# Kernel optimization log

Measured on AMD Instinct MI355X. Metric: run time of the kernel, lower is better.

## Reference

```python
import jax, jax.numpy as jnp
import numpy as np

N_EMBED = 768
N_HEAD = 12
SEQ = 4096
BATCH = 1
LN_EPS = 1e-5


def setup_inputs() -> dict:
    key = jax.random.key(0)
    ks = jax.random.split(key, 12)
    d = N_EMBED
    s = 0.02
    return {
        "x": jax.random.normal(ks[0], (BATCH, SEQ, d), jnp.float32),
        "w_qkv": jax.random.normal(ks[1], (d, 3 * d), jnp.float32) * s,
        "b_qkv": jnp.zeros((3 * d,), jnp.float32),
        "w_proj": jax.random.normal(ks[2], (d, d), jnp.float32) * s,
        "b_proj": jnp.zeros((d,), jnp.float32),
        "w_fc1": jax.random.normal(ks[3], (d, 4 * d), jnp.float32) * s,
        "b_fc1": jnp.zeros((4 * d,), jnp.float32),
        "w_fc2": jax.random.normal(ks[4], (4 * d, d), jnp.float32) * s,
        "b_fc2": jnp.zeros((d,), jnp.float32),
        "ln1_g": jnp.ones((d,), jnp.float32),
        "ln1_b": jnp.zeros((d,), jnp.float32),
        "ln2_g": jnp.ones((d,), jnp.float32),
        "ln2_b": jnp.zeros((d,), jnp.float32),
    }


def _layernorm(x, g, b):
    mu = jnp.mean(x, axis=-1, keepdims=True)
    var = jnp.mean(jnp.square(x - mu), axis=-1, keepdims=True)
    return (x - mu) * jax.lax.rsqrt(var + LN_EPS) * g + b


def _attn(x, w_qkv, b_qkv, w_proj, b_proj):
    B, S, D = x.shape
    hd = D // N_HEAD
    kqv = x @ w_qkv + b_qkv
    # torch order: k, q, v
    k, q, v = jnp.split(kqv, 3, axis=-1)
    def heads(t):
        return t.reshape(B, S, N_HEAD, hd).transpose(0, 2, 1, 3)  # [B,H,S,hd]
    k, q, v = heads(k), heads(q), heads(v)
    scores = jnp.einsum("bhqd,bhkd->bhqk", q, k) * (1.0 / jnp.sqrt(jnp.float32(hd)))
    causal = jnp.tril(jnp.ones((S, S), bool))
    scores = jnp.where(causal, scores, -jnp.inf)
    attn = jax.nn.softmax(scores, axis=-1)
    # dropout is identity in eval mode
    y = jnp.einsum("bhqk,bhkd->bhqd", attn, v)
    y = y.transpose(0, 2, 1, 3).reshape(B, S, D)
    return y @ w_proj + b_proj


def reference(x, w_qkv, b_qkv, w_proj, b_proj, w_fc1, b_fc1, w_fc2, b_fc2,
              ln1_g, ln1_b, ln2_g, ln2_b):
    x = x + _attn(_layernorm(x, ln1_g, ln1_b), w_qkv, b_qkv, w_proj, b_proj)
    h = _layernorm(x, ln2_g, ln2_b)
    h = jax.nn.gelu(h @ w_fc1 + b_fc1, approximate=False)
    return x + (h @ w_fc2 + b_fc2)
```

## Files before the change

### kernel.cpp

```cpp
#include <hip/hip_runtime.h>
#include <hip/hip_bf16.h>

#define S_LEN 4096
#define D_EMB 768
#define NH    12
#define HD    64
#define DQKV  2304
#define DFF   3072

typedef __attribute__((ext_vector_type(4))) short short4v;
typedef __attribute__((ext_vector_type(8))) short short8v;
typedef __attribute__((ext_vector_type(4))) float float4v;

static __device__ __forceinline__ float4v mfma16(short4v a, short4v b, float4v c) {
  return __builtin_amdgcn_mfma_f32_16x16x16bf16_1k(a, b, c, 0, 0, 0);
}

static __device__ __forceinline__ short bf16bits(float f) {
  __hip_bfloat16 h = __float2bfloat16(f);
  return *reinterpret_cast<short*>(&h);
}

static __device__ __forceinline__ float fast_exp2(float x) {
#if __has_builtin(__builtin_amdgcn_exp2f)
  return __builtin_amdgcn_exp2f(x);
#else
  return exp2f(x);
#endif
}

static __device__ __forceinline__ void gload16(const __hip_bfloat16* g, __hip_bfloat16* l) {
  __builtin_amdgcn_global_load_lds((const __attribute__((address_space(1))) void*)g,
                                   (__attribute__((address_space(3))) void*)l, 16, 0, 0);
}

__global__ __launch_bounds__(256) void ln_kernel(const float* __restrict__ x,
    const float* __restrict__ g, const float* __restrict__ b,
    __hip_bfloat16* __restrict__ out)
{
  int row = blockIdx.x;
  int tid = threadIdx.x;
  const float* xr = x + (size_t)row * D_EMB;
  float v0 = xr[tid], v1 = xr[tid + 256], v2 = xr[tid + 512];
  float s  = v0 + v1 + v2;
  float sq = v0 * v0 + v1 * v1 + v2 * v2;
  #pragma unroll
  for (int off = 32; off >= 1; off >>= 1) {
    s  += __shfl_xor(s, off);
    sq += __shfl_xor(sq, off);
  }
  __shared__ float ss[4], ssq[4];
  if ((tid & 63) == 0) { ss[tid >> 6] = s; ssq[tid >> 6] = sq; }
  __syncthreads();
  s  = ss[0] + ss[1] + ss[2] + ss[3];
  sq = ssq[0] + ssq[1] + ssq[2] + ssq[3];
  float mean = s * (1.0f / D_EMB);
  float var  = sq * (1.0f / D_EMB) - mean * mean;
  float rstd = rsqrtf(var + 1e-5f);
  __hip_bfloat16* orow = out + (size_t)row * D_EMB;
  orow[tid]       = __float2bfloat16((v0 - mean) * rstd * g[tid]       + b[tid]);
  orow[tid + 256] = __float2bfloat16((v1 - mean) * rstd * g[tid + 256] + b[tid + 256]);
  orow[tid + 512] = __float2bfloat16((v2 - mean) * rstd * g[tid + 512] + b[tid + 512]);
}

__global__ __launch_bounds__(256) void transpose_bf16_kernel(const float* __restrict__ in,
    __hip_bfloat16* __restrict__ out, int K, int N)
{
  __shared__ float t[32][33];
  int nb = N >> 5;
  int bn = blockIdx.x % nb, bk = blockIdx.x / nb;
  int tx = threadIdx.x & 31, ty = threadIdx.x >> 5;
  #pragma unroll
  for (int i = 0; i < 4; i++)
    t[ty + 8 * i][tx] = in[(size_t)(bk * 32 + ty + 8 * i) * N + bn * 32 + tx];
  __syncthreads();
  #pragma unroll
  for (int i = 0; i < 4; i++)
    out[(size_t)(bn * 32 + ty + 8 * i) * K + bk * 32 + tx] = __float2bfloat16(t[tx][ty + 8 * i]);
}

template<int EPI>
__global__ __launch_bounds__(256) void gemm_kernel(
    const __hip_bfloat16* __restrict__ A,
    const __hip_bfloat16* __restrict__ Bt,
    const float* __restrict__ bias,
    const float* __restrict__ resid,
    void* __restrict__ Cout,
    __hip_bfloat16* __restrict__ vtout,
    int M, int N, int Kfull, int kChunk)
{
  __shared__ __hip_bfloat16 Asm[128 * 64];
  __shared__ __hip_bfloat16 Bsm[128 * 64];
  int nb = N >> 7, mb = M >> 7;
  int tilesPer = nb * mb;
  int split = blockIdx.x / tilesPer;
  int b2 = blockIdx.x % tilesPer;
  int bx = b2 % nb, by = b2 / nb;
  int m0 = by << 7, n0 = bx << 7;
  int k0 = split * kChunk;
  int tid = threadIdx.x;
  int lane = tid & 63, lg = lane >> 4, li = lane & 15;
  int w = tid >> 6, wr = w >> 1, wc = w & 1;

  int sr  = tid >> 3;
  int scn = (tid & 7) ^ (sr & 7);
  const __hip_bfloat16* aSrc = A  + (size_t)(m0 + sr) * Kfull + k0 + scn * 8;
  const __hip_bfloat16* bSrc = Bt + (size_t)(n0 + sr) * Kfull + k0 + scn * 8;
  __hip_bfloat16* aDst = Asm + tid * 8;
  __hip_bfloat16* bDst = Bsm + tid * 8;
  const size_t rowStep = (size_t)32 * Kfull;

  float4v acc[4][4];
  #pragma unroll
  for (int i = 0; i < 4; i++)
    #pragma unroll
    for (int j = 0; j < 4; j++) {
      float4v z = {0.f, 0.f, 0.f, 0.f};
      acc[i][j] = z;
    }

  int sw = li & 7;

  for (int kt = 0; kt < kChunk; kt += 64) {
    #pragma unroll
    for (int i = 0; i < 4; i++) {
      gload16(aSrc + i * rowStep, aDst + i * 2048);
      gload16(bSrc + i * rowStep, bDst + i * 2048);
    }
    aSrc += 64; bSrc += 64;
    __syncthreads();
    #pragma unroll
    for (int kk = 0; kk < 2; kk++) {
      short8v af[4], bf[4];
      #pragma unroll
      for (int f = 0; f < 4; f++) {
        int ar = wr * 64 + f * 16 + li;
        int br = wc * 64 + f * 16 + li;
        int ch = ((kk << 2) | lg) ^ sw;
        af[f] = *(const short8v*)(Asm + ar * 64 + ch * 8);
        bf[f] = *(const short8v*)(Bsm + br * 64 + ch * 8);
      }
      #pragma unroll
      for (int fr = 0; fr < 4; fr++)
        #pragma unroll
        for (int fc = 0; fc < 4; fc++)
          acc[fr][fc] = __builtin_amdgcn_mfma_f32_16x16x32_bf16(af[fr], bf[fc], acc[fr][fc], 0, 0, 0);
    }
    __syncthreads();
  }

  #pragma unroll
  for (int fr = 0; fr < 4; fr++) {
    int row = m0 + wr * 64 + fr * 16 + lg * 4;
    #pragma unroll
    for (int fc = 0; fc < 4; fc++) {
      int col = n0 + wc * 64 + fc * 16 + li;
      float bv = (EPI == 3) ? 0.f : bias[col];
      short4v tv;
      #pragma unroll
      for (int r = 0; r < 4; r++) {
        float v = acc[fr][fc][r] + bv;
        size_t idx = (size_t)(row + r) * N + col;
        if (EPI == 1) {
          float u = 0.7978845608028654f * (v + 0.044715f * v * v * v);
          float e = fast_exp2(u * 2.8853900817779268f);
#if __has_builtin(__builtin_amdgcn_rcpf)
          float r1 = __builtin_amdgcn_rcpf(e + 1.0f);
#else
          float r1 = 1.0f / (e + 1.0f);
#endif
          v = v * e * r1;
          ((__hip_bfloat16*)Cout)[idx] = __float2bfloat16(v);
        } else if (EPI == 2) {
          ((float*)Cout)[idx] = v + resid[idx];
        } else if (EPI == 3) {
          ((__hip_bfloat16*)Cout)[(size_t)split * M * N + idx] = __float2bfloat16(v);
        } else {
          __hip_bfloat16 hb = __float2bfloat16(v);
          ((__hip_bfloat16*)Cout)[idx] = hb;
          if (EPI == 4) tv[r] = *reinterpret_cast<short*>(&hb);
        }
      }
      if (EPI == 4 && col >= 2 * D_EMB) {
        *reinterpret_cast<short4v*>(vtout + (size_t)(col - 2 * D_EMB) * S_LEN + row) = tv;
      }
    }
  }
}

template<int NS>
__global__ __launch_bounds__(256) void reduce_kernel(const __hip_bfloat16* __restrict__ parts,
    const float* __restrict__ bias, const float* __restrict__ resid,
    float* __restrict__ out, int n4)
{
  const size_t MN = (size_t)S_LEN * D_EMB;
  int stride = gridDim.x * 256;
  for (int e = blockIdx.x * 256 + threadIdx.x; e < n4; e += stride) {
    float4v acc = *(const float4v*)(resid + 4 * (size_t)e);
    int col = (e * 4) % D_EMB;
    float4v bv = *(const float4v*)(bias + col);
    acc += bv;
    #pragma unroll
    for (int s = 0; s < NS; s++) {
      short4v pv = *(const short4v*)(parts + (size_t)s * MN + 4 * (size_t)e);
      #pragma unroll
      for (int j = 0; j < 4; j++) {
        unsigned int u = ((unsigned int)(unsigned short)pv[j]) << 16;
        acc[j] += *reinterpret_cast<float*>(&u);
      }
    }
    *(float4v*)(out + 4 * (size_t)e) = acc;
  }
}

__global__ __launch_bounds__(256) void reduce_ln_kernel(const __hip_bfloat16* __restrict__ parts,
    const float* __restrict__ bias, const float* __restrict__ resid,
    const float* __restrict__ g, const float* __restrict__ b,
    float* __restrict__ x1, __hip_bfloat16* __restrict__ lnout)
{
  const size_t MN = (size_t)S_LEN * D_EMB;
  int row = blockIdx.x;
  int tid = threadIdx.x;
  float v[3];
  float s = 0.f, sq = 0.f;
  #pragma unroll
  for (int i = 0; i < 3; i++) {
    int col = tid + i * 256;
    size_t idx = (size_t)row * D_EMB + col;
    float a = resid[idx] + bias[col]
            + __bfloat162float(parts[idx])
            + __bfloat162float(parts[idx + MN])
            + __bfloat162float(parts[idx + 2 * MN]);
    x1[idx] = a;
    v[i] = a;
    s += a;
    sq += a * a;
  }
  #pragma unroll
  for (int off = 32; off >= 1; off >>= 1) {
    s  += __shfl_xor(s, off);
    sq += __shfl_xor(sq, off);
  }
  __shared__ float ss[4], ssq[4];
  if ((tid & 63) == 0) { ss[tid >> 6] = s; ssq[tid >> 6] = sq; }
  __syncthreads();
  s  = ss[0] + ss[1] + ss[2] + ss[3];
  sq = ssq[0] + ssq[1] + ssq[2] + ssq[3];
  float mean = s * (1.0f / D_EMB);
  float var  = sq * (1.0f / D_EMB) - mean * mean;
  float rstd = rsqrtf(var + 1e-5f);
  __hip_bfloat16* orow = lnout + (size_t)row * D_EMB;
  #pragma unroll
  for (int i = 0; i < 3; i++) {
    int col = tid + i * 256;
    orow[col] = __float2bfloat16((v[i] - mean) * rstd * g[col] + b[col]);
  }
}

#define SCL_LOG2E 0.18033688011f
template<bool SPLIT>
__global__ __launch_bounds__(512, 4) void attn_kernel(const __hip_bfloat16* __restrict__ kqv,
                                                      const __hip_bfloat16* __restrict__ vT,
                                                      __hip_bfloat16* __restrict__ y,
                                                      char* __restrict__ partial)
{
  __shared__ __hip_bfloat16 Ksm[2][64 * 64];
  __shared__ __hip_bfloat16 Vtsm[2][64 * 64];

  int bid = blockIdx.x;
  int h, gi, c;
  if (SPLIT) {
    int task = (bid >> 3) + (bid & 7) * 60;
    h = task / 40;
    int t = task % 40;
    if      (t < 16) { gi = 15 - (t >> 2);        c = t & 3; }
    else if (t < 28) { gi = 11 - (t - 16) / 3;    c = (t - 16) % 3; }
    else if (t < 36) { gi = 7  - ((t - 28) >> 1); c = (t - 28) & 1; }
    else             { gi = 3  - (t - 36);        c = 0; }
  } else {
    h = bid / 16; gi = 15 - (bid % 16); c = 0;
  }
  int ntile = 4 * gi + 4;
  int kt0 = c << 4;
  int kt1 = SPLIT ? min(kt0 + 16, ntile) : ntile;
  bool direct = SPLIT ? (gi < 4) : true;

  int tid = threadIdx.x;
  int w = tid >> 6, lane = tid & 63, lg = lane >> 4, li = lane & 15;
  int sw = li & 7;
  int qb0 = gi * 256 + w * 16;

  int ksr  = tid >> 3;
  int kscn = (tid & 7) ^ (ksr & 7);
  const __hip_bfloat16* kSrc0 = kqv + h * HD + (size_t)ksr * DQKV + kscn * 8;
  const __hip_bfloat16* vSrc0 = vT + (size_t)(h * HD + ksr) * S_LEN + kscn * 8;
  const size_t kTileStep = (size_t)64 * DQKV;

  short8v q8[2][2];
  #pragma unroll
  for (int g = 0; g < 2; g++) {
    const __hip_bfloat16* qp = kqv + (size_t)(qb0 + g * 128 + li) * DQKV + D_EMB + h * HD + 8 * lg;
    q8[g][0] = *(const short8v*)(qp);
    q8[g][1] = *(const short8v*)(qp + 32);
  }

  const short4v ones4 = { (short)0x3F80, (short)0x3F80, (short)0x3F80, (short)0x3F80 };
  float4v ol0 = {0.f,0.f,0.f,0.f}, ol1 = {0.f,0.f,0.f,0.f};
  float4v o0[4], o1[4];
  #pragma unroll
  for (int fc = 0; fc < 4; fc++) { float4v z = {0.f,0.f,0.f,0.f}; o0[fc] = z; o1[fc] = z; }

  gload16(kSrc0 + (size_t)kt0 * kTileStep, Ksm[0] + tid * 8);
  gload16(vSrc0 + (size_t)kt0 * 64,        Vtsm[0] + tid * 8);

  for (int kb = kt0; kb < kt1; kb++) {
    int p = kb & 1;
    __syncthreads();
    if (kb + 1 < kt1) {
      gload16(kSrc0 + (size_t)(kb + 1) * kTileStep, Ksm[p ^ 1] + tid * 8);
      gload16(vSrc0 + (size_t)(kb + 1) * 64,        Vtsm[p ^ 1] + tid * 8);
    }

    bool act0 = (kb * 64 <= qb0 + 15);
    bool act1 = (kb * 64 <= qb0 + 128 + 15);
    if (!act1) continue;

    float4v s0[4], s1[4];
    #pragma unroll
    for (int fc = 0; fc < 4; fc++) { float4v z = {0.f,0.f,0.f,0.f}; s0[fc] = z; s1[fc] = z; }
    #pragma unroll
    for (int kk = 0; kk < 2; kk++) {
      #pragma unroll
      for (int fc = 0; fc < 4; fc++) {
        int ch = ((kk << 2) | lg) ^ sw;
        short8v kf = *(const short8v*)(Ksm[p] + (fc * 16 + li) * 64 + ch * 8);
        s0[fc] = __builtin_amdgcn_mfma_f32_16x16x32_bf16(kf, q8[0][kk], s0[fc], 0, 0, 0);
        s1[fc] = __builtin_amdgcn_mfma_f32_16x16x32_bf16(kf, q8[1][kk], s1[fc], 0, 0, 0);
      }
    }

    if (act0) {
      bool needmask = (kb * 64 + 63 > qb0);
      if (needmask) {
        #pragma unroll
        for (int fc = 0; fc < 4; fc++) {
          #pragma unroll
          for (int rr = 0; rr < 4; rr++) {
            float pv = fast_exp2(s0[fc][rr] * SCL_LOG2E);
            if ((kb * 64 + fc * 16 + 4 * lg + rr) > (qb0 + li)) pv = 0.f;
            s0[fc][rr] = pv;
          }
        }
      } else {
        #pragma unroll
        for (int fc = 0; fc < 4; fc++) {
          #pragma unroll
          for (int rr = 0; rr < 4; rr++)
            s0[fc][rr] = fast_exp2(s0[fc][rr] * SCL_LOG2E);
        }
      }
    }

    {
      int qb1 = qb0 + 128;
      bool needmask = (kb * 64 + 63 > qb1);
      if (needmask) {
        #pragma unroll
        for (int fc = 0; fc < 4; fc++) {
          #pragma unroll
          for (int rr = 0; rr < 4; rr++) {
            float pv = fast_exp2(s1[fc][rr] * SCL_LOG2E);
            if ((kb * 64 + fc * 16 + 4 * lg + rr) > (qb1 + li)) pv = 0.f;
            s1[fc][rr] = pv;
          }
        }
      } else {
        #pragma unroll
        for (int fc = 0; fc < 4; fc++) {
          #pragma unroll
          for (int rr = 0; rr < 4; rr++)
            s1[fc][rr] = fast_exp2(s1[fc][rr] * SCL_LOG2E);
        }
      }
    }

    if (act0) {
      #pragma unroll
      for (int kk = 0; kk < 4; kk++) {
        short4v pb0, pb1;
        #pragma unroll
        for (int rr = 0; rr < 4; rr++) { pb0[rr] = bf16bits(s0[kk][rr]); pb1[rr] = bf16bits(s1[kk][rr]); }
        ol0 = mfma16(ones4, pb0, ol0);
        ol1 = mfma16(ones4, pb1, ol1);
        int c2 = (kk << 1) | (lg >> 1);
        #pragma unroll
        for (int fc = 0; fc < 4; fc++) {
          short4v vf = *(const short4v*)(Vtsm[p] + (fc * 16 + li) * 64 + ((c2 ^ sw) << 3) + 4 * (lg & 1));
          o0[fc] = mfma16(vf, pb0, o0[fc]);
          o1[fc] = mfma16(vf, pb1, o1[fc]);
        }
      }
    } else {
      #pragma unroll
      for (int kk = 0; kk < 4; kk++) {
        short4v pb1;
        #pragma unroll
        for (int rr = 0; rr < 4; rr++) pb1[rr] = bf16bits(s1[kk][rr]);
        ol1 = mfma16(ones4, pb1, ol1);
        int c2 = (kk << 1) | (lg >> 1);
        #pragma unroll
        for (int fc = 0; fc < 4; fc++) {
          short4v vf = *(const short4v*)(Vtsm[p] + (fc * 16 + li) * 64 + ((c2 ^ sw) << 3) + 4 * (lg & 1));
          o1[fc] = mfma16(vf, pb1, o1[fc]);
        }
      }
    }
  }

  if (direct) {
    float inv0 = 1.0f / ol0[0], inv1 = 1.0f / ol1[0];
    int q0 = qb0 + li;
    #pragma unroll
    for (int fc = 0; fc < 4; fc++) {
      short4v ov0, ov1;
      #pragma unroll
      for (int rr = 0; rr < 4; rr++) { ov0[rr] = bf16bits(o0[fc][rr] * inv0); ov1[rr] = bf16bits(o1[fc][rr] * inv1); }
      *reinterpret_cast<short4v*>(y + (size_t)q0 * D_EMB + h * HD + fc * 16 + 4 * lg) = ov0;
      *reinterpret_cast<short4v*>(y + (size_t)(q0 + 128) * D_EMB + h * HD + fc * 16 + 4 * lg) = ov1;
    }
  } else {
    int offg = (gi < 8) ? (gi - 4) * 2 : (gi < 12) ? 8 + (gi - 8) * 3 : 20 + (gi - 12) * 4;
    char* slot = partial + (size_t)(h * 36 + offg + c) * 33792;
    int q = (w & 3) * 16 + li;
    #pragma unroll
    for (int g = 0; g < 2; g++) {
      char* ps = slot + (size_t)(g * 2 + (w >> 2)) * 8448;
      __hip_bfloat16* pO = (__hip_bfloat16*)ps;
      float* pL = (float*)(ps + 8192);
      #pragma unroll
      for (int fc = 0; fc < 4; fc++) {
        #pragma unroll
        for (int rr = 0; rr < 4; rr++) {
          float val = g ? o1[fc][rr] : o0[fc][rr];
          pO[(fc * 16 + 4 * lg + rr) * 64 + q] = __float2bfloat16(val);
        }
      }
      if (lg == 0) pL[q] = g ? ol1[0] : ol0[0];
    }
  }
}

__global__ __launch_bounds__(256) void attn_combine_kernel(const char* __restrict__ partial,
                                                           __hip_bfloat16* __restrict__ y)
{
  int task = blockIdx.x;
  int h  = task / 48;
  int qb = 16 + task % 48;
  int gi = qb >> 2, slab = qb & 3;
  int nch = (gi >> 2) + 1;
  int offg = (gi < 8) ? (gi - 4) * 2 : (gi < 12) ? 8 + (gi - 8) * 3 : 20 + (gi - 12) * 4;
  const char* base = partial + (size_t)(h * 36 + offg) * 33792 + (size_t)slab * 8448;
  int wv = threadIdx.x >> 6;
  int lane = threadIdx.x & 63;

  float L = 0.f;
  float acc[16];
  #pragma unroll
  for (int j = 0; j < 16; j++) acc[j] = 0.f;
  #pragma unroll
  for (int c = 0; c < 4; c++) {
    if (c < nch) {
      const char* cb = base + (size_t)c * 33792;
      L += ((const float*)(cb + 8192))[lane];
      const __hip_bfloat16* O = (const __hip_bfloat16*)cb;
      #pragma unroll
      for (int j = 0; j < 16; j++)
        acc[j] += __bfloat162float(O[(wv * 16 + j) * 64 + lane]);
    }
  }
  float inv = 1.0f / L;
  __hip_bfloat16* yp = y + (size_t)(qb * 64 + lane) * D_EMB + h * HD + wv * 16;
  short8v a0, a1;
  #pragma unroll
  for (int j = 0; j < 8; j++) a0[j] = bf16bits(acc[j] * inv);
  #pragma unroll
  for (int j = 0; j < 8; j++) a1[j] = bf16bits(acc[8 + j] * inv);
  *reinterpret_cast<short8v*>(yp)     = a0;
  *reinterpret_cast<short8v*>(yp + 8) = a1;
}

extern "C" void kernel_launch(void* const* d_in, const int* in_sizes, int n_in,
                              void* d_out, int out_size, void* d_ws, size_t ws_size,
                              hipStream_t stream)
{
  const float* x      = (const float*)d_in[0];
  const float* w_qkv  = (const float*)d_in[1];
  const float* b_qkv  = (const float*)d_in[2];
  const float* w_proj = (const float*)d_in[3];
  const float* b_proj = (const float*)d_in[4];
  const float* w_fc1  = (const float*)d_in[5];
  const float* b_fc1  = (const float*)d_in[6];
  const float* w_fc2  = (const float*)d_in[7];
  const float* b_fc2  = (const float*)d_in[8];
  const float* ln1_g  = (const float*)d_in[9];
  const float* ln1_b  = (const float*)d_in[10];
  const float* ln2_g  = (const float*)d_in[11];
  const float* ln2_b  = (const float*)d_in[12];

  char* ws = (char*)d_ws;
  size_t off = 0;
  __hip_bfloat16* wqkvT = (__hip_bfloat16*)(ws + off); off += (size_t)DQKV * D_EMB * 2;
  __hip_bfloat16* wprojT= (__hip_bfloat16*)(ws + off); off += (size_t)D_EMB * D_EMB * 2;
  __hip_bfloat16* wfc1T = (__hip_bfloat16*)(ws + off); off += (size_t)DFF * D_EMB * 2;
  __hip_bfloat16* wfc2T = (__hip_bfloat16*)(ws + off); off += (size_t)D_EMB * DFF * 2;
  __hip_bfloat16* lnbuf = (__hip_bfloat16*)(ws + off); off += (size_t)S_LEN * D_EMB * 2;
  __hip_bfloat16* kqv   = (__hip_bfloat16*)(ws + off);
  __hip_bfloat16* hbuf  = kqv;                         off += (size_t)S_LEN * DQKV * 2;
  __hip_bfloat16* ybuf  = (__hip_bfloat16*)(ws + off); off += (size_t)S_LEN * D_EMB * 2;
  __hip_bfloat16* vTbuf = (__hip_bfloat16*)(ws + off); off += (size_t)S_LEN * D_EMB * 2;
  float*          x1    = (float*)(ws + off);          off += (size_t)S_LEN * D_EMB * 4;
  char*           part  = ws + off;
  size_t needSplit = off + (size_t)4 * S_LEN * D_EMB * 2;
  size_t needAttn  = off + (size_t)432 * 33792;
  bool splitk  = (ws_size >= needSplit);
  bool attnSpl = (ws_size >= needAttn);
  const int MN4 = S_LEN * D_EMB / 4;
  (void)in_sizes; (void)n_in; (void)out_size;

  transpose_bf16_kernel<<<dim3((DQKV/32)*(D_EMB/32)), dim3(256), 0, stream>>>(w_qkv,  wqkvT, D_EMB, DQKV);
  transpose_bf16_kernel<<<dim3((D_EMB/32)*(D_EMB/32)), dim3(256), 0, stream>>>(w_proj, wprojT, D_EMB, D_EMB);
  transpose_bf16_kernel<<<dim3((DFF/32)*(D_EMB/32)),   dim3(256), 0, stream>>>(w_fc1,  wfc1T, D_EMB, DFF);
  transpose_bf16_kernel<<<dim3((D_EMB/32)*(DFF/32)),   dim3(256), 0, stream>>>(w_fc2,  wfc2T, DFF, D_EMB);

  ln_kernel<<<dim3(S_LEN), dim3(256), 0, stream>>>(x, ln1_g, ln1_b, lnbuf);
  gemm_kernel<4><<<dim3((DQKV/128)*(S_LEN/128)), dim3(256), 0, stream>>>(
      lnbuf, wqkvT, b_qkv, nullptr, kqv, vTbuf, S_LEN, DQKV, D_EMB, D_EMB);

  if (attnSpl) {
    attn_kernel<true><<<dim3(480), dim3(512), 0, stream>>>(kqv, vTbuf, ybuf, part);
    attn_combine_kernel<<<dim3(576), dim3(256), 0, stream>>>(part, ybuf);
  } else {
    attn_kernel<false><<<dim3(192), dim3(512), 0, stream>>>(kqv, vTbuf, ybuf, part);
  }

  if (splitk) {
    gemm_kernel<3><<<dim3((D_EMB/128)*(S_LEN/128)*3), dim3(256), 0, stream>>>(
        ybuf, wprojT, nullptr, nullptr, part, nullptr, S_LEN, D_EMB, D_EMB, D_EMB/3);
    reduce_ln_kernel<<<dim3(S_LEN), dim3(256), 0, stream>>>(
        (const __hip_bfloat16*)part, b_proj, x, ln2_g, ln2_b, x1, lnbuf);
  } else {
    gemm_kernel<2><<<dim3((D_EMB/128)*(S_LEN/128)), dim3(256), 0, stream>>>(
        ybuf, wprojT, b_proj, x, x1, nullptr, S_LEN, D_EMB, D_EMB, D_EMB);
    ln_kernel<<<dim3(S_LEN), dim3(256), 0, stream>>>(x1, ln2_g, ln2_b, lnbuf);
  }

  gemm_kernel<1><<<dim3((DFF/128)*(S_LEN/128)), dim3(256), 0, stream>>>(
      lnbuf, wfc1T, b_fc1, nullptr, hbuf, nullptr, S_LEN, DFF, D_EMB, D_EMB);

  if (splitk) {
    gemm_kernel<3><<<dim3((D_EMB/128)*(S_LEN/128)*4), dim3(256), 0, stream>>>(
        hbuf, wfc2T, nullptr, nullptr, part, nullptr, S_LEN, D_EMB, DFF, DFF/4);
    reduce_kernel<4><<<dim3(1024), dim3(256), 0, stream>>>(
        (const __hip_bfloat16*)part, b_fc2, x1, (float*)d_out, MN4);
  } else {
    gemm_kernel<2><<<dim3((D_EMB/128)*(S_LEN/128)), dim3(256), 0, stream>>>(
        hbuf, wfc2T, b_fc2, x1, (float*)d_out, nullptr, S_LEN, D_EMB, DFF, DFF);
  }
}
```

Measured before the change: 188.1 us.

## Double-buffer GEMM LDS tiles, merge weight transposes, add MFMA priority hints

```diff
diff --git a/kernel.cpp b/kernel.cpp
--- a/kernel.cpp
+++ b/kernel.cpp
@@ -63,12 +63,21 @@
   orow[tid + 512] = __float2bfloat16((v2 - mean) * rstd * g[tid + 512] + b[tid + 512]);
 }
 
-__global__ __launch_bounds__(256) void transpose_bf16_kernel(const float* __restrict__ in,
-    __hip_bfloat16* __restrict__ out, int K, int N)
+__global__ __launch_bounds__(256) void transpose_all_kernel(
+    const float* __restrict__ w_qkv, const float* __restrict__ w_proj,
+    const float* __restrict__ w_fc1, const float* __restrict__ w_fc2,
+    __hip_bfloat16* __restrict__ wqkvT, __hip_bfloat16* __restrict__ wprojT,
+    __hip_bfloat16* __restrict__ wfc1T, __hip_bfloat16* __restrict__ wfc2T)
 {
   __shared__ float t[32][33];
+  int bid = blockIdx.x;
+  const float* in; __hip_bfloat16* out; int K, N, tt;
+  if (bid < 1728)      { in = w_qkv;  out = wqkvT;  K = D_EMB; N = DQKV;  tt = bid; }
+  else if (bid < 2304) { in = w_proj; out = wprojT; K = D_EMB; N = D_EMB; tt = bid - 1728; }
+  else if (bid < 4608) { in = w_fc1;  out = wfc1T;  K = D_EMB; N = DFF;   tt = bid - 2304; }
+  else                 { in = w_fc2;  out = wfc2T;  K = DFF;   N = D_EMB; tt = bid - 4608; }
   int nb = N >> 5;
-  int bn = blockIdx.x % nb, bk = blockIdx.x / nb;
+  int bn = tt % nb, bk = tt / nb;
   int tx = threadIdx.x & 31, ty = threadIdx.x >> 5;
   #pragma unroll
   for (int i = 0; i < 4; i++)
@@ -89,8 +98,8 @@
     __hip_bfloat16* __restrict__ vtout,
     int M, int N, int Kfull, int kChunk)
 {
-  __shared__ __hip_bfloat16 Asm[128 * 64];
-  __shared__ __hip_bfloat16 Bsm[128 * 64];
+  __shared__ __hip_bfloat16 Asm[2][128 * 32];
+  __shared__ __hip_bfloat16 Bsm[2][128 * 32];
   int nb = N >> 7, mb = M >> 7;
   int tilesPer = nb * mb;
   int split = blockIdx.x / tilesPer;
@@ -102,13 +111,11 @@
   int lane = tid & 63, lg = lane >> 4, li = lane & 15;
   int w = tid >> 6, wr = w >> 1, wc = w & 1;
 
-  int sr  = tid >> 3;
-  int scn = (tid & 7) ^ (sr & 7);
+  int sr  = tid >> 2;
+  int scn = (tid & 3) ^ ((tid >> 3) & 3);
   const __hip_bfloat16* aSrc = A  + (size_t)(m0 + sr) * Kfull + k0 + scn * 8;
   const __hip_bfloat16* bSrc = Bt + (size_t)(n0 + sr) * Kfull + k0 + scn * 8;
-  __hip_bfloat16* aDst = Asm + tid * 8;
-  __hip_bfloat16* bDst = Bsm + tid * 8;
-  const size_t rowStep = (size_t)32 * Kfull;
+  const size_t rowStep = (size_t)64 * Kfull;
 
   float4v acc[4][4];
   #pragma unroll
@@ -119,34 +126,36 @@
       acc[i][j] = z;
     }
 
-  int sw = li & 7;
-
-  for (int kt = 0; kt < kChunk; kt += 64) {
-    #pragma unroll
-    for (int i = 0; i < 4; i++) {
-      gload16(aSrc + i * rowStep, aDst + i * 2048);
-      gload16(bSrc + i * rowStep, bDst + i * 2048);
-    }
-    aSrc += 64; bSrc += 64;
+  int ch = lg ^ ((li >> 1) & 3);
+  int nk = kChunk >> 5;
+
+  gload16(aSrc,           Asm[0] + tid * 8);
+  gload16(aSrc + rowStep, Asm[0] + tid * 8 + 2048);
+  gload16(bSrc,           Bsm[0] + tid * 8);
+  gload16(bSrc + rowStep, Bsm[0] + tid * 8 + 2048);
+  aSrc += 32; bSrc += 32;
+
+  for (int t = 0; t < nk; ++t) {
+    int p = t & 1;
     __syncthreads();
-    #pragma unroll
-    for (int kk = 0; kk < 2; kk++) {
-      short8v af[4], bf[4];
-      #pragma unroll
-      for (int f = 0; f < 4; f++) {
-        int ar = wr * 64 + f * 16 + li;
-        int br = wc * 64 + f * 16 + li;
-        int ch = ((kk << 2) | lg) ^ sw;
-        af[f] = *(const short8v*)(Asm + ar * 64 + ch * 8);
-        bf[f] = *(const short8v*)(Bsm + br * 64 + ch * 8);
-      }
-      #pragma unroll
-      for (int fr = 0; fr < 4; fr++)
-        #pragma unroll
-        for (int fc = 0; fc < 4; fc++)
-          acc[fr][fc] = __builtin_amdgcn_mfma_f32_16x16x32_bf16(af[fr], bf[fc], acc[fr][fc], 0, 0, 0);
-    }
-    __syncthreads();
+    if (t + 1 < nk) {
+      gload16(aSrc,           Asm[p ^ 1] + tid * 8);
+      gload16(aSrc + rowStep, Asm[p ^ 1] + tid * 8 + 2048);
+      gload16(bSrc,           Bsm[p ^ 1] + tid * 8);
+      gload16(bSrc + rowStep, Bsm[p ^ 1] + tid * 8 + 2048);
+      aSrc += 32; bSrc += 32;
+    }
+    short8v af[4], bf[4];
+    #pragma unroll
+    for (int f = 0; f < 4; f++) {
+      af[f] = *(const short8v*)(Asm[p] + (wr * 64 + f * 16 + li) * 32 + ch * 8);
+      bf[f] = *(const short8v*)(Bsm[p] + (wc * 64 + f * 16 + li) * 32 + ch * 8);
+    }
+    #pragma unroll
+    for (int fr = 0; fr < 4; fr++)
+      #pragma unroll
+      for (int fc = 0; fc < 4; fc++)
+        acc[fr][fc] = __builtin_amdgcn_mfma_f32_16x16x32_bf16(af[fr], bf[fc], acc[fr][fc], 0, 0, 0);
   }
 
   #pragma unroll
@@ -328,6 +337,7 @@
     float4v s0[4], s1[4];
     #pragma unroll
     for (int fc = 0; fc < 4; fc++) { float4v z = {0.f,0.f,0.f,0.f}; s0[fc] = z; s1[fc] = z; }
+    __builtin_amdgcn_s_setprio(1);
     #pragma unroll
     for (int kk = 0; kk < 2; kk++) {
       #pragma unroll
@@ -338,6 +348,7 @@
         s1[fc] = __builtin_amdgcn_mfma_f32_16x16x32_bf16(kf, q8[1][kk], s1[fc], 0, 0, 0);
       }
     }
+    __builtin_amdgcn_s_setprio(0);
 
     if (act0) {
       bool needmask = (kb * 64 + 63 > qb0);
@@ -384,6 +395,7 @@
       }
     }
 
+    __builtin_amdgcn_s_setprio(1);
     if (act0) {
       #pragma unroll
       for (int kk = 0; kk < 4; kk++) {
@@ -415,6 +427,7 @@
         }
       }
     }
+    __builtin_amdgcn_s_setprio(0);
   }
 
   if (direct) {
@@ -527,10 +540,8 @@
   const int MN4 = S_LEN * D_EMB / 4;
   (void)in_sizes; (void)n_in; (void)out_size;
 
-  transpose_bf16_kernel<<<dim3((DQKV/32)*(D_EMB/32)), dim3(256), 0, stream>>>(w_qkv,  wqkvT, D_EMB, DQKV);
-  transpose_bf16_kernel<<<dim3((D_EMB/32)*(D_EMB/32)), dim3(256), 0, stream>>>(w_proj, wprojT, D_EMB, D_EMB);
-  transpose_bf16_kernel<<<dim3((DFF/32)*(D_EMB/32)),   dim3(256), 0, stream>>>(w_fc1,  wfc1T, D_EMB, DFF);
-  transpose_bf16_kernel<<<dim3((D_EMB/32)*(DFF/32)),   dim3(256), 0, stream>>>(w_fc2,  wfc2T, DFF, D_EMB);
+  transpose_all_kernel<<<dim3(6912), dim3(256), 0, stream>>>(
+      w_qkv, w_proj, w_fc1, w_fc2, wqkvT, wprojT, wfc1T, wfc2T);
 
   ln_kernel<<<dim3(S_LEN), dim3(256), 0, stream>>>(x, ln1_g, ln1_b, lnbuf);
   gemm_kernel<4><<<dim3((DQKV/128)*(S_LEN/128)), dim3(256), 0, stream>>>(
```

Result: no change. 191.4 us (+1.8%).
